# Kernel optimization log

Hardware: AMD Instinct MI355X
Metric: run time of the kernel (lower is better)

## Reference

```python
import jax, jax.numpy as jnp
import numpy as np

N = 100000   # nodes
E = 1000000  # edges
IN = 100     # input feature dim
H = 4        # heads
D = 32       # hidden per head (H*D = 128)
C = 47       # classes
EPS = 1e-5
SLOPE = 0.2  # DGL GATv2 leaky_relu negative slope


def setup_inputs() -> dict:
    key = jax.random.key(0)
    ks = jax.random.split(key, 32)
    lin = lambda k, i, o: (jax.random.normal(k, (i, o), jnp.float32) / np.float32(np.sqrt(i)))
    inp = {}
    inp['x'] = jax.random.normal(ks[0], (N, IN), jnp.float32)
    inp['src'] = jax.random.randint(ks[1], (E,), 0, N, jnp.int32)
    inp['dst'] = jnp.sort(jax.random.randint(ks[2], (E,), 0, N, jnp.int32))
    # layer 0: IN -> H*D, Linear residual (IN != H*D)
    inp['Wsrc0'] = lin(ks[3], IN, H * D); inp['bsrc0'] = jnp.zeros(H * D, jnp.float32)
    inp['Wdst0'] = lin(ks[4], IN, H * D); inp['bdst0'] = jnp.zeros(H * D, jnp.float32)
    inp['attn0'] = lin(ks[5], H, D)
    inp['Wres0'] = lin(ks[6], IN, H * D); inp['bres0'] = jnp.zeros(H * D, jnp.float32)
    # layer 1: H*D -> H*D, Identity residual (128 == 128)
    inp['Wsrc1'] = lin(ks[7], H * D, H * D); inp['bsrc1'] = jnp.zeros(H * D, jnp.float32)
    inp['Wdst1'] = lin(ks[8], H * D, H * D); inp['bdst1'] = jnp.zeros(H * D, jnp.float32)
    inp['attn1'] = lin(ks[9], H, D)
    # layer 2: H*D -> H*C, Linear residual (128 != 188)
    inp['Wsrc2'] = lin(ks[10], H * D, H * C); inp['bsrc2'] = jnp.zeros(H * C, jnp.float32)
    inp['Wdst2'] = lin(ks[11], H * D, H * C); inp['bdst2'] = jnp.zeros(H * C, jnp.float32)
    inp['attn2'] = lin(ks[12], H, C)
    inp['Wres2'] = lin(ks[13], H * D, H * C); inp['bres2'] = jnp.zeros(H * C, jnp.float32)
    # BatchNorm1d params (training-mode batch stats)
    inp['g0'] = jnp.ones(H * D, jnp.float32); inp['be0'] = jnp.zeros(H * D, jnp.float32)
    inp['g1'] = jnp.ones(H * D, jnp.float32); inp['be1'] = jnp.zeros(H * D, jnp.float32)
    return inp


def _gatv2(h, src, dst, Ws, bs, Wd, bd, attn, resval):
    """One GATv2Conv on a full block (src feats == dst feats == h)."""
    Hh, Dd = attn.shape
    fs = (h @ Ws + bs).reshape(-1, Hh, Dd)   # [N,H,D] src projection
    fd = (h @ Wd + bd).reshape(-1, Hh, Dd)   # [N,H,D] dst projection
    e = jax.nn.leaky_relu(fs[src] + fd[dst], SLOPE)         # [E,H,D]
    logits = jnp.einsum('ehd,hd->eh', e, attn)              # [E,H]
    m = jax.ops.segment_max(logits, dst, num_segments=N)    # per-dst max
    ex = jnp.exp(logits - m[dst])
    s = jax.ops.segment_sum(ex, dst, num_segments=N)
    alpha = ex / s[dst]                                      # edge softmax
    out = jax.ops.segment_sum(alpha[:, :, None] * fs[src], dst, num_segments=N)
    return out + resval                                      # [N,H,D]


def _bn(x, g, b):
    mu = x.mean(0)
    v = x.var(0)  # biased, as torch BN training mode
    return g * (x - mu) / jnp.sqrt(v + EPS) + b


def reference(x, src, dst,
              Wsrc0, bsrc0, Wdst0, bdst0, attn0, Wres0, bres0,
              Wsrc1, bsrc1, Wdst1, bdst1, attn1,
              Wsrc2, bsrc2, Wdst2, bdst2, attn2, Wres2, bres2,
              g0, be0, g1, be1):
    # layer 0: conv(+relu activation) -> flatten -> BN -> relu (dropout = eval identity)
    res0 = (x @ Wres0 + bres0).reshape(N, H, D)
    h = jax.nn.relu(_gatv2(x, src, dst, Wsrc0, bsrc0, Wdst0, bdst0, attn0, res0))
    h = jax.nn.relu(_bn(h.reshape(N, H * D), g0, be0))
    # layer 1: Identity residual
    res1 = h.reshape(N, H, D)
    h = jax.nn.relu(_gatv2(h, src, dst, Wsrc1, bsrc1, Wdst1, bdst1, attn1, res1))
    h = jax.nn.relu(_bn(h.reshape(N, H * D), g1, be1))
    # layer 2: no activation; mean over heads; log_softmax
    res2 = (h @ Wres2 + bres2).reshape(N, H, C)
    h = _gatv2(h, src, dst, Wsrc2, bsrc2, Wdst2, bdst2, attn2, res2)
    h = h.mean(1)                                # [N,C]
    return jax.nn.log_softmax(h, axis=-1)
```

## Files before the change

kernel.cpp:

```cpp
#include <hip/hip_runtime.h>
#include <hip/hip_bf16.h>

#define Nn 100000
#define Ee 1000000
#define INF_ 100
#define Hh 4
#define Dd 32
#define HD 128
#define Cc 47
#define HC 188
#define EPSV 1e-5f
#define SLOPE 0.2f

typedef __hip_bfloat16 bf16;
typedef __attribute__((ext_vector_type(8))) short short8;
typedef __attribute__((ext_vector_type(4))) float f32x4;

__device__ __forceinline__ float tof(bf16 v) { return __bfloat162float(v); }
__device__ __forceinline__ float b2f(unsigned short u) {
    return __uint_as_float((unsigned)u << 16);
}
__device__ __forceinline__ float ldb(const bf16* p) {
    return b2f(*(const unsigned short*)p);
}
__device__ __forceinline__ unsigned short f2u(float v) {
    bf16 t = __float2bfloat16(v);
    return *(unsigned short*)&t;
}

__global__ void detect_dtype(const unsigned* __restrict__ x, int* __restrict__ flag) {
    if (blockIdx.x == 0 && threadIdx.x == 0) {
        int good = 0;
        for (int i = 0; i < 256; ++i) {
            unsigned lo = x[i] & 0xFFFFu;
            float v = __uint_as_float(lo << 16);
            float a = fabsf(v);
            if (a > 1e-4f && a < 10.f) good++;
        }
        *flag = (good >= 128) ? 1 : 0;
    }
}

__device__ __forceinline__ float ld_any(const void* p, int i, int isbf) {
    return isbf ? tof(((const bf16*)p)[i]) : ((const float*)p)[i];
}

__global__ void cvt_x(const void* __restrict__ in, bf16* __restrict__ out,
                      const int* __restrict__ flag) {
    int i = blockIdx.x * blockDim.x + threadIdx.x;
    if (i >= Nn * 128) return;
    int row = i >> 7, col = i & 127;
    float v = (col < INF_) ? ld_any(in, row * INF_ + col, *flag) : 0.f;
    out[i] = __float2bfloat16(v);
}

#define NSP 15
struct CvtTab { const void* src[NSP]; int off[NSP + 1]; };

__global__ void cvt_params(CvtTab t, bf16* __restrict__ out, int total,
                           const int* __restrict__ flag) {
    int i = blockIdx.x * blockDim.x + threadIdx.x;
    if (i >= total) return;
    int isbf = *flag;
    int seg = 0;
    while (i >= t.off[seg + 1]) seg++;
    out[i] = __float2bfloat16(ld_any(t.src[seg], i - t.off[seg], isbf));
}

#define WROWS 1280
struct PrepTab { const void* src[8]; int row0[8]; int K[8]; int M[8]; int MP[8]; };

__global__ void prep_all(PrepTab t, bf16* __restrict__ wtb, const int* __restrict__ flag) {
    int i = blockIdx.x * blockDim.x + threadIdx.x;
    if (i >= WROWS * 128) return;
    int row = i >> 7, k = i & 127;
    int isbf = *flag;
    float v = 0.f;
#pragma unroll
    for (int q = 0; q < 8; ++q) {
        if (row >= t.row0[q] && row < t.row0[q] + t.MP[q]) {
            int m = row - t.row0[q];
            if (m < t.M[q] && k < t.K[q])
                v = ld_any(t.src[q], k * t.M[q] + m, isbf);
        }
    }
    wtb[i] = __float2bfloat16(v);
}

__global__ void zero_u32(unsigned* __restrict__ p, int n) {
    int i = blockIdx.x * blockDim.x + threadIdx.x;
    if (i < n) p[i] = 0u;
}

__global__ void build_ptr(const int* __restrict__ dst, int* __restrict__ ptr) {
    int n = blockIdx.x * blockDim.x + threadIdx.x;
    if (n > Nn) return;
    if (n == Nn) { ptr[Nn] = Ee; return; }
    int lo = 0, hi = Ee;
    while (lo < hi) {
        int mid = (lo + hi) >> 1;
        if (dst[mid] < n) lo = mid + 1; else hi = mid;
    }
    ptr[n] = lo;
}

template <int MP, int NOUT, int CS, bool ABN>
__global__ __launch_bounds__(256, 4) void gemm_big(
    const bf16* __restrict__ A, const bf16* __restrict__ Wt,
    const bf16* __restrict__ b0, const bf16* __restrict__ b1,
    const bf16* __restrict__ b2,
    bf16* __restrict__ o0, bf16* __restrict__ o1, bf16* __restrict__ o2,
    int MR, const float* __restrict__ bnp) {
    __shared__ __align__(16) bf16 Al[64 * 136];
    const int row0 = blockIdx.x * 64;
    const int tid = threadIdx.x;
#pragma unroll
    for (int j = 0; j < 4; ++j) {
        int idx = tid + j * 256;
        int r = idx >> 4, kk = (idx & 15) * 8;
        int4 val = {0, 0, 0, 0};
        if (row0 + r < Nn) {
            val = *(const int4*)&A[(size_t)(row0 + r) * 128 + kk];
            if (ABN) {
                short8 av = *(short8*)&val;
                bf16 tmp[8];
#pragma unroll
                for (int u = 0; u < 8; ++u) {
                    float v = b2f((unsigned short)av[u]);
                    v = fmaxf(fmaf(v, bnp[kk + u], bnp[128 + kk + u]), 0.f);
                    tmp[u] = __float2bfloat16(v);
                }
                val = *(int4*)tmp;
            }
        }
        *(int4*)&Al[r * 136 + kk] = val;
    }
    __syncthreads();
    const int wave = tid >> 6, lane = tid & 63;
    const int n16 = lane & 15, quad = lane >> 4;
    const int colbase = blockIdx.y * (64 * CS) + wave * (16 * CS);
    f32x4 acc[4][CS];
#pragma unroll
    for (int rt = 0; rt < 4; ++rt)
#pragma unroll
        for (int c = 0; c < CS; ++c) acc[rt][c] = (f32x4){0.f, 0.f, 0.f, 0.f};
    const bf16* wb[CS];
#pragma unroll
    for (int c = 0; c < CS; ++c)
        wb[c] = Wt + (size_t)(colbase + c * 16 + n16) * 128 + quad * 8;
    const bf16* ap = Al + n16 * 136 + quad * 8;
#pragma unroll
    for (int ks = 0; ks < 4; ++ks) {
        short8 bf[CS];
#pragma unroll
        for (int c = 0; c < CS; ++c) bf[c] = *(const short8*)(wb[c] + ks * 32);
#pragma unroll
        for (int rt = 0; rt < 4; ++rt) {
            short8 af = *(const short8*)(ap + rt * 16 * 136 + ks * 32);
#pragma unroll
            for (int c = 0; c < CS; ++c)
                acc[rt][c] = __builtin_amdgcn_mfma_f32_16x16x32_bf16(af, bf[c], acc[rt][c], 0, 0, 0);
        }
    }
#pragma unroll
    for (int c = 0; c < CS; ++c) {
        int col = colbase + c * 16 + n16;
        int oi = col / MP, lc = col - oi * MP;
        if (oi >= NOUT || lc >= MR) continue;
        const bf16* bp = (oi == 0) ? b0 : (oi == 1) ? b1 : b2;
        bf16* o = (oi == 0) ? o0 : (oi == 1) ? o1 : o2;
        float bb = tof(bp[lc]);
#pragma unroll
        for (int rt = 0; rt < 4; ++rt) {
#pragma unroll
            for (int i = 0; i < 4; ++i) {
                int row = row0 + rt * 16 + quad * 4 + i;
                if (row < Nn)
                    o[(size_t)row * MR + lc] = __float2bfloat16(acc[rt][c][i] + bb);
            }
        }
    }
}

template <bool RESBN>
__global__ __launch_bounds__(256) void gat_fused_128(
    const bf16* __restrict__ fs, const bf16* __restrict__ fd,
    const int* __restrict__ srcI, const int* __restrict__ ptr,
    const bf16* __restrict__ attn, const bf16* __restrict__ resb,
    const float* __restrict__ bnp, bf16* __restrict__ hout) {
    const int wave = threadIdx.x >> 6, lane = threadIdx.x & 63;
    const int d = blockIdx.x * 4 + wave;
    if (d >= Nn) return;
    const int c0 = lane * 2;
    ushort2 aq = *(const ushort2*)&attn[c0];
    float a0 = b2f(aq.x), a1 = b2f(aq.y);
    ushort2 dq = *(const ushort2*)&fd[(size_t)d * HD + c0];
    float fd0 = b2f(dq.x), fd1 = b2f(dq.y);
    float m = -INFINITY, l = 0.f, O0 = 0.f, O1 = 0.f;
    int e = ptr[d];
    const int e1 = ptr[d + 1];
    for (; e + 1 < e1; e += 2) {
        int sa = srcI[e], sb = srcI[e + 1];
        ushort2 qa = *(const ushort2*)&fs[(size_t)sa * HD + c0];
        ushort2 qb = *(const ushort2*)&fs[(size_t)sb * HD + c0];
        float fa0 = b2f(qa.x), fa1 = b2f(qa.y);
        float fb0 = b2f(qb.x), fb1 = b2f(qb.y);
        float ta0 = fa0 + fd0; ta0 = fmaxf(ta0, ta0 * SLOPE);
        float ta1 = fa1 + fd1; ta1 = fmaxf(ta1, ta1 * SLOPE);
        float tb0 = fb0 + fd0; tb0 = fmaxf(tb0, tb0 * SLOPE);
        float tb1 = fb1 + fd1; tb1 = fmaxf(tb1, tb1 * SLOPE);
        float pa = fmaf(ta0, a0, ta1 * a1);
        float pb = fmaf(tb0, a0, tb1 * a1);
        pa += __shfl_xor(pa, 1); pb += __shfl_xor(pb, 1);
        pa += __shfl_xor(pa, 2); pb += __shfl_xor(pb, 2);
        pa += __shfl_xor(pa, 4); pb += __shfl_xor(pb, 4);
        pa += __shfl_xor(pa, 8); pb += __shfl_xor(pb, 8);
        float mn = fmaxf(m, fmaxf(pa, pb));
        float sc = __expf(m - mn);
        float ea = __expf(pa - mn), eb = __expf(pb - mn);
        l = fmaf(l, sc, ea + eb);
        O0 = fmaf(O0, sc, fmaf(ea, fa0, eb * fb0));
        O1 = fmaf(O1, sc, fmaf(ea, fa1, eb * fb1));
        m = mn;
    }
    if (e < e1) {
        int s = srcI[e];
        ushort2 fq = *(const ushort2*)&fs[(size_t)s * HD + c0];
        float f0 = b2f(fq.x), f1 = b2f(fq.y);
        float t0 = f0 + fd0; t0 = fmaxf(t0, t0 * SLOPE);
        float t1 = f1 + fd1; t1 = fmaxf(t1, t1 * SLOPE);
        float p = fmaf(t0, a0, t1 * a1);
        p += __shfl_xor(p, 1); p += __shfl_xor(p, 2);
        p += __shfl_xor(p, 4); p += __shfl_xor(p, 8);
        float mn = fmaxf(m, p);
        float sc = __expf(m - mn);
        float pe = __expf(p - mn);
        l = fmaf(l, sc, pe);
        O0 = fmaf(O0, sc, pe * f0);
        O1 = fmaf(O1, sc, pe * f1);
    }
    float inv = l > 0.f ? 1.f / l : 0.f;
    ushort2 rq = *(const ushort2*)&resb[(size_t)d * HD + c0];
    float r0 = b2f(rq.x), r1 = b2f(rq.y);
    if (RESBN) {
        r0 = fmaxf(fmaf(r0, bnp[c0], bnp[HD + c0]), 0.f);
        r1 = fmaxf(fmaf(r1, bnp[c0 + 1], bnp[HD + c0 + 1]), 0.f);
    }
    float v0 = fmaxf(fmaf(O0, inv, r0), 0.f);
    float v1 = fmaxf(fmaf(O1, inv, r1), 0.f);
    ushort2 ov; ov.x = f2u(v0); ov.y = f2u(v1);
    *(ushort2*)&hout[(size_t)d * HD + c0] = ov;
}

__global__ __launch_bounds__(256) void gat_fused_188(
    const bf16* __restrict__ fs, const bf16* __restrict__ fd,
    const int* __restrict__ srcI, const int* __restrict__ ptr,
    const bf16* __restrict__ attn, const bf16* __restrict__ rs,
    void* __restrict__ out, const int* __restrict__ flag) {
    const int wave = threadIdx.x >> 6, lane = threadIdx.x & 63;
    const int d = blockIdx.x * 4 + wave;
    if (d >= Nn) return;
    const int h = lane >> 4, j = lane & 15;
    const int c0 = h * Cc + j;
    const bool has2 = (j < 15);
    float a0 = ldb(&attn[c0]);
    float a1 = ldb(&attn[c0 + 16]);
    float a2 = has2 ? ldb(&attn[c0 + 32]) : 0.f;
    const bf16* fdr = fd + (size_t)d * HC;
    float fd0 = ldb(&fdr[c0]);
    float fd1 = ldb(&fdr[c0 + 16]);
    float fd2 = has2 ? ldb(&fdr[c0 + 32]) : 0.f;
    float m = -INFINITY, l = 0.f, O0 = 0.f, O1 = 0.f, O2 = 0.f;
    int e = ptr[d];
    const int e1 = ptr[d + 1];
    for (; e + 1 < e1; e += 2) {
        int sa = srcI[e], sb = srcI[e + 1];
        const bf16* fra = fs + (size_t)sa * HC;
        const bf16* frb = fs + (size_t)sb * HC;
        float fa0 = ldb(&fra[c0]), fb0 = ldb(&frb[c0]);
        float fa1 = ldb(&fra[c0 + 16]), fb1 = ldb(&frb[c0 + 16]);
        float fa2 = has2 ? ldb(&fra[c0 + 32]) : 0.f;
        float fb2 = has2 ? ldb(&frb[c0 + 32]) : 0.f;
        float ta0 = fa0 + fd0; ta0 = fmaxf(ta0, ta0 * SLOPE);
        float ta1 = fa1 + fd1; ta1 = fmaxf(ta1, ta1 * SLOPE);
        float ta2 = fa2 + fd2; ta2 = fmaxf(ta2, ta2 * SLOPE);
        float tb0 = fb0 + fd0; tb0 = fmaxf(tb0, tb0 * SLOPE);
        float tb1 = fb1 + fd1; tb1 = fmaxf(tb1, tb1 * SLOPE);
        float tb2 = fb2 + fd2; tb2 = fmaxf(tb2, tb2 * SLOPE);
        float pa = fmaf(ta0, a0, fmaf(ta1, a1, ta2 * a2));
        float pb = fmaf(tb0, a0, fmaf(tb1, a1, tb2 * a2));
        pa += __shfl_xor(pa, 1); pb += __shfl_xor(pb, 1);
        pa += __shfl_xor(pa, 2); pb += __shfl_xor(pb, 2);
        pa += __shfl_xor(pa, 4); pb += __shfl_xor(pb, 4);
        pa += __shfl_xor(pa, 8); pb += __shfl_xor(pb, 8);
        float mn = fmaxf(m, fmaxf(pa, pb));
        float sc = __expf(m - mn);
        float ea = __expf(pa - mn), eb = __expf(pb - mn);
        l = fmaf(l, sc, ea + eb);
        O0 = fmaf(O0, sc, fmaf(ea, fa0, eb * fb0));
        O1 = fmaf(O1, sc, fmaf(ea, fa1, eb * fb1));
        O2 = fmaf(O2, sc, fmaf(ea, fa2, eb * fb2));
        m = mn;
    }
    if (e < e1) {
        int s = srcI[e];
        const bf16* fr = fs + (size_t)s * HC;
        float f0 = ldb(&fr[c0]);
        float f1 = ldb(&fr[c0 + 16]);
        float f2 = has2 ? ldb(&fr[c0 + 32]) : 0.f;
        float t0 = f0 + fd0; t0 = fmaxf(t0, t0 * SLOPE);
        float t1 = f1 + fd1; t1 = fmaxf(t1, t1 * SLOPE);
        float t2 = f2 + fd2; t2 = fmaxf(t2, t2 * SLOPE);
        float p = fmaf(t0, a0, fmaf(t1, a1, t2 * a2));
        p += __shfl_xor(p, 1); p += __shfl_xor(p, 2);
        p += __shfl_xor(p, 4); p += __shfl_xor(p, 8);
        float mn = fmaxf(m, p);
        float sc = __expf(m - mn);
        float pe = __expf(p - mn);
        l = fmaf(l, sc, pe);
        O0 = fmaf(O0, sc, pe * f0);
        O1 = fmaf(O1, sc, pe * f1);
        O2 = fmaf(O2, sc, pe * f2);
    }
    float inv = l > 0.f ? 1.f / l : 0.f;
    const bf16* rr = rs + (size_t)d * HC;
    float v0 = fmaf(O0, inv, ldb(&rr[c0]));
    float v1 = fmaf(O1, inv, ldb(&rr[c0 + 16]));
    float v2 = has2 ? fmaf(O2, inv, ldb(&rr[c0 + 32])) : 0.f;
    v0 += __shfl_xor(v0, 16); v0 += __shfl_xor(v0, 32); v0 *= 0.25f;
    v1 += __shfl_xor(v1, 16); v1 += __shfl_xor(v1, 32); v1 *= 0.25f;
    v2 += __shfl_xor(v2, 16); v2 += __shfl_xor(v2, 32); v2 *= 0.25f;
    float mx = fmaxf(v0, v1);
    if (has2) mx = fmaxf(mx, v2);
    mx = fmaxf(mx, __shfl_xor(mx, 1)); mx = fmaxf(mx, __shfl_xor(mx, 2));
    mx = fmaxf(mx, __shfl_xor(mx, 4)); mx = fmaxf(mx, __shfl_xor(mx, 8));
    float sm = __expf(v0 - mx) + __expf(v1 - mx) + (has2 ? __expf(v2 - mx) : 0.f);
    sm += __shfl_xor(sm, 1); sm += __shfl_xor(sm, 2);
    sm += __shfl_xor(sm, 4); sm += __shfl_xor(sm, 8);
    if (h == 0) {
        float ls = mx + logf(sm);
        if (*flag) {
            bf16* o = (bf16*)out + (size_t)d * Cc;
            o[j] = __float2bfloat16(v0 - ls);
            o[j + 16] = __float2bfloat16(v1 - ls);
            if (has2) o[j + 32] = __float2bfloat16(v2 - ls);
        } else {
            float* o = (float*)out + (size_t)d * Cc;
            o[j] = v0 - ls;
            o[j + 16] = v1 - ls;
            if (has2) o[j + 32] = v2 - ls;
        }
    }
}

__global__ void col_stats(const bf16* __restrict__ in, float* __restrict__ sums) {
    int c = threadIdx.x;
    int r0 = blockIdx.x * 256;
    int r1 = r0 + 256; if (r1 > Nn) r1 = Nn;
    float s = 0.f, s2 = 0.f;
    for (int r = r0; r < r1; ++r) {
        float v = ldb(&in[(size_t)r * HD + c]);
        s += v; s2 += v * v;
    }
    atomicAdd(&sums[c], s);
    atomicAdd(&sums[HD + c], s2);
}

__global__ void bn_finalize(const float* __restrict__ sums, const bf16* __restrict__ g,
                            const bf16* __restrict__ be, float* __restrict__ ss) {
    int c = threadIdx.x;
    float mu = sums[c] * (1.f / Nn);
    float var = sums[HD + c] * (1.f / Nn) - mu * mu;
    float sc = tof(g[c]) * rsqrtf(var + EPSV);
    ss[c] = sc;
    ss[HD + c] = tof(be[c]) - mu * sc;
}

extern "C" void kernel_launch(void* const* d_in, const int* in_sizes, int n_in,
                              void* d_out, int out_size, void* d_ws, size_t ws_size,
                              hipStream_t stream) {
    (void)in_sizes; (void)n_in; (void)out_size; (void)ws_size;
    const void* x = d_in[0];
    const int* src = (const int*)d_in[1];
    const int* dst = (const int*)d_in[2];

    char* ws = (char*)d_ws;
    size_t off = 0;
    auto alloc = [&](size_t bytes) {
        void* p = ws + off;
        off += (bytes + 255) & ~(size_t)255;
        return p;
    };
    bf16* xb = (bf16*)alloc((size_t)Nn * 128 * 2);
    bf16* rb = (bf16*)alloc((size_t)Nn * HD * 2);
    bf16* rs = xb;
    bf16* fs = (bf16*)alloc((size_t)Nn * HC * 2);
    bf16* fd = (bf16*)alloc((size_t)Nn * HC * 2);
    bf16* hbA = (bf16*)alloc((size_t)Nn * HD * 2);
    bf16* hbB = (bf16*)alloc((size_t)Nn * HD * 2);
    int* ptr = (int*)alloc((Nn + 1) * 4);
    bf16* wtb = (bf16*)alloc((size_t)WROWS * 128 * 2);
    float* bns = (float*)alloc(2 * HD * 4);
    float* bnss0 = (float*)alloc(2 * HD * 4);
    float* bnss1 = (float*)alloc(2 * HD * 4);
    bf16* pb = (bf16*)alloc(4096 * 2);
    int* flag = (int*)alloc(256);

    static const int spIdx[NSP] = {4, 6, 7, 9, 11, 13, 14, 16, 18, 19, 21, 22, 23, 24, 25};
    static const int spSz[NSP]  = {HD, HD, HD, HD, HD, HD, HD, HC, HC, HC, HC, HD, HD, HD, HD};
    CvtTab tab;
    int tot = 0;
    for (int i = 0; i < NSP; ++i) { tab.src[i] = d_in[spIdx[i]]; tab.off[i] = tot; tot += spSz[i]; }
    tab.off[NSP] = tot;
    const bf16 *bsrc0 = pb + tab.off[0], *bdst0 = pb + tab.off[1], *attn0 = pb + tab.off[2],
               *bres0 = pb + tab.off[3], *bsrc1 = pb + tab.off[4], *bdst1 = pb + tab.off[5],
               *attn1 = pb + tab.off[6], *bsrc2 = pb + tab.off[7], *bdst2 = pb + tab.off[8],
               *attn2 = pb + tab.off[9], *bres2 = pb + tab.off[10],
               *g0 = pb + tab.off[11], *be0 = pb + tab.off[12],
               *g1 = pb + tab.off[13], *be1 = pb + tab.off[14];

    PrepTab pt;
    static const int wIdx[8] = {3, 5, 8, 10, 12, 15, 17, 20};
    static const int wK[8]   = {INF_, INF_, INF_, HD, HD, HD, HD, HD};
    static const int wM[8]   = {HD, HD, HD, HD, HD, HC, HC, HC};
    static const int wMP[8]  = {128, 128, 128, 128, 128, 192, 192, 192};
    static const int wR0[8]  = {0, 128, 256, 384, 512, 640, 832, 1024};
    for (int i = 0; i < 8; ++i) {
        pt.src[i] = d_in[wIdx[i]]; pt.row0[i] = wR0[i];
        pt.K[i] = wK[i]; pt.M[i] = wM[i]; pt.MP[i] = wMP[i];
    }

    detect_dtype<<<1, 64, 0, stream>>>((const unsigned*)x, flag);
    cvt_x<<<(Nn * 128 + 255) / 256, 256, 0, stream>>>(x, xb, flag);
    cvt_params<<<(tot + 255) / 256, 256, 0, stream>>>(tab, pb, tot, flag);
    prep_all<<<(WROWS * 128 + 255) / 256, 256, 0, stream>>>(pt, wtb, flag);
    build_ptr<<<(Nn + 256) / 256, 256, 0, stream>>>(dst, ptr);

    const int fusedGrid = (Nn + 3) / 4;
    const int statsGrid = (Nn + 255) / 256;
    const int rowBlk = (Nn + 63) / 64;

    gemm_big<128, 3, 2, false><<<dim3(rowBlk, 3), 256, 0, stream>>>(
        xb, wtb, bsrc0, bdst0, bres0, fs, fd, rb, HD, nullptr);
    gat_fused_128<false><<<fusedGrid, 256, 0, stream>>>(fs, fd, src, ptr, attn0,
                                                        rb, nullptr, hbA);
    zero_u32<<<1, 256, 0, stream>>>((unsigned*)bns, 2 * HD);
    col_stats<<<statsGrid, 128, 0, stream>>>(hbA, bns);
    bn_finalize<<<1, HD, 0, stream>>>(bns, g0, be0, bnss0);

    gemm_big<128, 2, 2, true><<<dim3(rowBlk, 2), 256, 0, stream>>>(
        hbA, wtb + (size_t)384 * 128, bsrc1, bdst1, nullptr, fs, fd, nullptr, HD, bnss0);
    gat_fused_128<true><<<fusedGrid, 256, 0, stream>>>(fs, fd, src, ptr, attn1,
                                                       hbA, bnss0, hbB);
    zero_u32<<<1, 256, 0, stream>>>((unsigned*)bns, 2 * HD);
    col_stats<<<statsGrid, 128, 0, stream>>>(hbB, bns);
    bn_finalize<<<1, HD, 0, stream>>>(bns, g1, be1, bnss1);

    gemm_big<192, 3, 3, true><<<dim3(rowBlk, 3), 256, 0, stream>>>(
        hbB, wtb + (size_t)640 * 128, bsrc2, bdst2, bres2, fs, fd, rs, HC, bnss1);
    gat_fused_188<<<fusedGrid, 256, 0, stream>>>(fs, fd, src, ptr, attn2, rs,
                                                 d_out, flag);
}
```

Baseline: 744.9 us.

## Drop online-softmax max tracking, unroll gather by 4, replace BN atomics with partials

Removes the running-max rescaling in all GAT aggregation kernels and exponentiates the raw logits directly. This cuts exp and FMA work per edge but risks overflow if logits grow large. Unrolls the 128-wide edge loop to four edges per iteration for more memory-level parallelism. Replaces the atomic BN column stats and their zeroing kernel with per-block partials reduced serially in bn_finalize, and changes the first GEMM's template and grid configuration.

Result: slower. 901.6 us (+21.0%).

```diff
diff --git a/kernel.cpp b/kernel.cpp
--- a/kernel.cpp
+++ b/kernel.cpp
@@ -85,11 +85,6 @@
         }
     }
     wtb[i] = __float2bfloat16(v);
-}
-
-__global__ void zero_u32(unsigned* __restrict__ p, int n) {
-    int i = blockIdx.x * blockDim.x + threadIdx.x;
-    if (i < n) p[i] = 0u;
 }
 
 __global__ void build_ptr(const int* __restrict__ dst, int* __restrict__ ptr) {
@@ -196,34 +191,47 @@
     float a0 = b2f(aq.x), a1 = b2f(aq.y);
     ushort2 dq = *(const ushort2*)&fd[(size_t)d * HD + c0];
     float fd0 = b2f(dq.x), fd1 = b2f(dq.y);
-    float m = -INFINITY, l = 0.f, O0 = 0.f, O1 = 0.f;
+    float l = 0.f, O0 = 0.f, O1 = 0.f;
     int e = ptr[d];
     const int e1 = ptr[d + 1];
-    for (; e + 1 < e1; e += 2) {
-        int sa = srcI[e], sb = srcI[e + 1];
-        ushort2 qa = *(const ushort2*)&fs[(size_t)sa * HD + c0];
-        ushort2 qb = *(const ushort2*)&fs[(size_t)sb * HD + c0];
-        float fa0 = b2f(qa.x), fa1 = b2f(qa.y);
-        float fb0 = b2f(qb.x), fb1 = b2f(qb.y);
-        float ta0 = fa0 + fd0; ta0 = fmaxf(ta0, ta0 * SLOPE);
-        float ta1 = fa1 + fd1; ta1 = fmaxf(ta1, ta1 * SLOPE);
-        float tb0 = fb0 + fd0; tb0 = fmaxf(tb0, tb0 * SLOPE);
-        float tb1 = fb1 + fd1; tb1 = fmaxf(tb1, tb1 * SLOPE);
-        float pa = fmaf(ta0, a0, ta1 * a1);
-        float pb = fmaf(tb0, a0, tb1 * a1);
-        pa += __shfl_xor(pa, 1); pb += __shfl_xor(pb, 1);
-        pa += __shfl_xor(pa, 2); pb += __shfl_xor(pb, 2);
-        pa += __shfl_xor(pa, 4); pb += __shfl_xor(pb, 4);
-        pa += __shfl_xor(pa, 8); pb += __shfl_xor(pb, 8);
-        float mn = fmaxf(m, fmaxf(pa, pb));
-        float sc = __expf(m - mn);
-        float ea = __expf(pa - mn), eb = __expf(pb - mn);
-        l = fmaf(l, sc, ea + eb);
-        O0 = fmaf(O0, sc, fmaf(ea, fa0, eb * fb0));
-        O1 = fmaf(O1, sc, fmaf(ea, fa1, eb * fb1));
-        m = mn;
-    }
-    if (e < e1) {
+    for (; e + 3 < e1; e += 4) {
+        int sA = srcI[e], sB = srcI[e + 1], sC = srcI[e + 2], sD = srcI[e + 3];
+        ushort2 qA = *(const ushort2*)&fs[(size_t)sA * HD + c0];
+        ushort2 qB = *(const ushort2*)&fs[(size_t)sB * HD + c0];
+        ushort2 qC = *(const ushort2*)&fs[(size_t)sC * HD + c0];
+        ushort2 qD = *(const ushort2*)&fs[(size_t)sD * HD + c0];
+        float fA0 = b2f(qA.x), fA1 = b2f(qA.y);
+        float fB0 = b2f(qB.x), fB1 = b2f(qB.y);
+        float fC0 = b2f(qC.x), fC1 = b2f(qC.y);
+        float fD0 = b2f(qD.x), fD1 = b2f(qD.y);
+        float tA0 = fA0 + fd0; tA0 = fmaxf(tA0, tA0 * SLOPE);
+        float tA1 = fA1 + fd1; tA1 = fmaxf(tA1, tA1 * SLOPE);
+        float tB0 = fB0 + fd0; tB0 = fmaxf(tB0, tB0 * SLOPE);
+        float tB1 = fB1 + fd1; tB1 = fmaxf(tB1, tB1 * SLOPE);
+        float tC0 = fC0 + fd0; tC0 = fmaxf(tC0, tC0 * SLOPE);
+        float tC1 = fC1 + fd1; tC1 = fmaxf(tC1, tC1 * SLOPE);
+        float tD0 = fD0 + fd0; tD0 = fmaxf(tD0, tD0 * SLOPE);
+        float tD1 = fD1 + fd1; tD1 = fmaxf(tD1, tD1 * SLOPE);
+        float pA = fmaf(tA0, a0, tA1 * a1);
+        float pB = fmaf(tB0, a0, tB1 * a1);
+        float pC = fmaf(tC0, a0, tC1 * a1);
+        float pD = fmaf(tD0, a0, tD1 * a1);
+        pA += __shfl_xor(pA, 1); pB += __shfl_xor(pB, 1);
+        pC += __shfl_xor(pC, 1); pD += __shfl_xor(pD, 1);
+        pA += __shfl_xor(pA, 2); pB += __shfl_xor(pB, 2);
+        pC += __shfl_xor(pC, 2); pD += __shfl_xor(pD, 2);
+        pA += __shfl_xor(pA, 4); pB += __shfl_xor(pB, 4);
+        pC += __shfl_xor(pC, 4); pD += __shfl_xor(pD, 4);
+        pA += __shfl_xor(pA, 8); pB += __shfl_xor(pB, 8);
+        pC += __shfl_xor(pC, 8); pD += __shfl_xor(pD, 8);
+        float eA = __expf(pA), eB = __expf(pB), eC = __expf(pC), eD = __expf(pD);
+        l += (eA + eB) + (eC + eD);
+        O0 = fmaf(eA, fA0, O0); O0 = fmaf(eB, fB0, O0);
+        O0 = fmaf(eC, fC0, O0); O0 = fmaf(eD, fD0, O0);
+        O1 = fmaf(eA, fA1, O1); O1 = fmaf(eB, fB1, O1);
+        O1 = fmaf(eC, fC1, O1); O1 = fmaf(eD, fD1, O1);
+    }
+    for (; e < e1; ++e) {
         int s = srcI[e];
         ushort2 fq = *(const ushort2*)&fs[(size_t)s * HD + c0];
         float f0 = b2f(fq.x), f1 = b2f(fq.y);
@@ -232,12 +240,10 @@
         float p = fmaf(t0, a0, t1 * a1);
         p += __shfl_xor(p, 1); p += __shfl_xor(p, 2);
         p += __shfl_xor(p, 4); p += __shfl_xor(p, 8);
-        float mn = fmaxf(m, p);
-        float sc = __expf(m - mn);
-        float pe = __expf(p - mn);
-        l = fmaf(l, sc, pe);
-        O0 = fmaf(O0, sc, pe * f0);
-        O1 = fmaf(O1, sc, pe * f1);
+        float pe = __expf(p);
+        l += pe;
+        O0 = fmaf(pe, f0, O0);
+        O1 = fmaf(pe, f1, O1);
     }
     float inv = l > 0.f ? 1.f / l : 0.f;
     ushort2 rq = *(const ushort2*)&resb[(size_t)d * HD + c0];
@@ -270,7 +276,7 @@
     float fd0 = ldb(&fdr[c0]);
     float fd1 = ldb(&fdr[c0 + 16]);
     float fd2 = has2 ? ldb(&fdr[c0 + 32]) : 0.f;
-    float m = -INFINITY, l = 0.f, O0 = 0.f, O1 = 0.f, O2 = 0.f;
+    float l = 0.f, O0 = 0.f, O1 = 0.f, O2 = 0.f;
     int e = ptr[d];
     const int e1 = ptr[d + 1];
     for (; e + 1 < e1; e += 2) {
@@ -293,14 +299,11 @@
         pa += __shfl_xor(pa, 2); pb += __shfl_xor(pb, 2);
         pa += __shfl_xor(pa, 4); pb += __shfl_xor(pb, 4);
         pa += __shfl_xor(pa, 8); pb += __shfl_xor(pb, 8);
-        float mn = fmaxf(m, fmaxf(pa, pb));
-        float sc = __expf(m - mn);
-        float ea = __expf(pa - mn), eb = __expf(pb - mn);
-        l = fmaf(l, sc, ea + eb);
-        O0 = fmaf(O0, sc, fmaf(ea, fa0, eb * fb0));
-        O1 = fmaf(O1, sc, fmaf(ea, fa1, eb * fb1));
-        O2 = fmaf(O2, sc, fmaf(ea, fa2, eb * fb2));
-        m = mn;
+        float ea = __expf(pa), eb = __expf(pb);
+        l += ea + eb;
+        O0 = fmaf(ea, fa0, O0); O0 = fmaf(eb, fb0, O0);
+        O1 = fmaf(ea, fa1, O1); O1 = fmaf(eb, fb1, O1);
+        O2 = fmaf(ea, fa2, O2); O2 = fmaf(eb, fb2, O2);
     }
     if (e < e1) {
         int s = srcI[e];
@@ -314,13 +317,11 @@
         float p = fmaf(t0, a0, fmaf(t1, a1, t2 * a2));
         p += __shfl_xor(p, 1); p += __shfl_xor(p, 2);
         p += __shfl_xor(p, 4); p += __shfl_xor(p, 8);
-        float mn = fmaxf(m, p);
-        float sc = __expf(m - mn);
-        float pe = __expf(p - mn);
-        l = fmaf(l, sc, pe);
-        O0 = fmaf(O0, sc, pe * f0);
-        O1 = fmaf(O1, sc, pe * f1);
-        O2 = fmaf(O2, sc, pe * f2);
+        float pe = __expf(p);
+        l += pe;
+        O0 = fmaf(pe, f0, O0);
+        O1 = fmaf(pe, f1, O1);
+        O2 = fmaf(pe, f2, O2);
     }
     float inv = l > 0.f ? 1.f / l : 0.f;
     const bf16* rr = rs + (size_t)d * HC;
@@ -353,7 +354,7 @@
     }
 }
 
-__global__ void col_stats(const bf16* __restrict__ in, float* __restrict__ sums) {
+__global__ void col_stats(const bf16* __restrict__ in, float* __restrict__ partial) {
     int c = threadIdx.x;
     int r0 = blockIdx.x * 256;
     int r1 = r0 + 256; if (r1 > Nn) r1 = Nn;
@@ -362,15 +363,21 @@
         float v = ldb(&in[(size_t)r * HD + c]);
         s += v; s2 += v * v;
     }
-    atomicAdd(&sums[c], s);
-    atomicAdd(&sums[HD + c], s2);
-}
-
-__global__ void bn_finalize(const float* __restrict__ sums, const bf16* __restrict__ g,
-                            const bf16* __restrict__ be, float* __restrict__ ss) {
+    partial[blockIdx.x * 256 + c] = s;
+    partial[blockIdx.x * 256 + 128 + c] = s2;
+}
+
+__global__ void bn_finalize(const float* __restrict__ partial, int nb,
+                            const bf16* __restrict__ g, const bf16* __restrict__ be,
+                            float* __restrict__ ss) {
     int c = threadIdx.x;
-    float mu = sums[c] * (1.f / Nn);
-    float var = sums[HD + c] * (1.f / Nn) - mu * mu;
+    float s = 0.f, s2 = 0.f;
+    for (int b = 0; b < nb; ++b) {
+        s += partial[b * 256 + c];
+        s2 += partial[b * 256 + 128 + c];
+    }
+    float mu = s * (1.f / Nn);
+    float var = s2 * (1.f / Nn) - mu * mu;
     float sc = tof(g[c]) * rsqrtf(var + EPSV);
     ss[c] = sc;
     ss[HD + c] = tof(be[c]) - mu * sc;
@@ -400,7 +407,8 @@
     bf16* hbB = (bf16*)alloc((size_t)Nn * HD * 2);
     int* ptr = (int*)alloc((Nn + 1) * 4);
     bf16* wtb = (bf16*)alloc((size_t)WROWS * 128 * 2);
-    float* bns = (float*)alloc(2 * HD * 4);
+    const int statsGrid = (Nn + 255) / 256;
+    float* bnp_part = (float*)alloc((size_t)statsGrid * 256 * 4);
     float* bnss0 = (float*)alloc(2 * HD * 4);
     float* bnss1 = (float*)alloc(2 * HD * 4);
     bf16* pb = (bf16*)alloc(4096 * 2);
@@ -437,24 +445,21 @@
     build_ptr<<<(Nn + 256) / 256, 256, 0, stream>>>(dst, ptr);
 
     const int fusedGrid = (Nn + 3) / 4;
-    const int statsGrid = (Nn + 255) / 256;
     const int rowBlk = (Nn + 63) / 64;
 
-    gemm_big<128, 3, 2, false><<<dim3(rowBlk, 3), 256, 0, stream>>>(
+    gemm_big<128, 3, 3, false><<<dim3(rowBlk, 2), 256, 0, stream>>>(
         xb, wtb, bsrc0, bdst0, bres0, fs, fd, rb, HD, nullptr);
     gat_fused_128<false><<<fusedGrid, 256, 0, stream>>>(fs, fd, src, ptr, attn0,
                                                         rb, nullptr, hbA);
-    zero_u32<<<1, 256, 0, stream>>>((unsigned*)bns, 2 * HD);
-    col_stats<<<statsGrid, 128, 0, stream>>>(hbA, bns);
-    bn_finalize<<<1, HD, 0, stream>>>(bns, g0, be0, bnss0);
+    col_stats<<<statsGrid, 128, 0, stream>>>(hbA, bnp_part);
+    bn_finalize<<<1, HD, 0, stream>>>(bnp_part, statsGrid, g0, be0, bnss0);
 
     gemm_big<128, 2, 2, true><<<dim3(rowBlk, 2), 256, 0, stream>>>(
         hbA, wtb + (size_t)384 * 128, bsrc1, bdst1, nullptr, fs, fd, nullptr, HD, bnss0);
     gat_fused_128<true><<<fusedGrid, 256, 0, stream>>>(fs, fd, src, ptr, attn1,
                                                        hbA, bnss0, hbB);
-    zero_u32<<<1, 256, 0, stream>>>((unsigned*)bns, 2 * HD);
-    col_stats<<<statsGrid, 128, 0, stream>>>(hbB, bns);
-    bn_finalize<<<1, HD, 0, stream>>>(bns, g1, be1, bnss1);
+    col_stats<<<statsGrid, 128, 0, stream>>>(hbB, bnp_part);
+    bn_finalize<<<1, HD, 0, stream>>>(bnp_part, statsGrid, g1, be1, bnss1);
 
     gemm_big<192, 3, 3, true><<<dim3(rowBlk, 3), 256, 0, stream>>>(
         hbB, wtb + (size_t)640 * 128, bsrc2, bdst2, bres2, fs, fd, rs, HC, bnss1);
```
